# Kernel optimization log

Measured on AMD Instinct MI355X. Metric: run time of the kernel, lower is better.

## Reference

```python
import jax, jax.numpy as jnp
import numpy as np

DIM = 1024
MULTIPLE_OF = 256
NUM_EXPERTS = 8
TOP_K = 2
T = 2048  # flattened tokens


def _hidden_dim(dim: int, multiple_of: int) -> int:
    h = 4 * dim
    h = int(2 * h / 3)
    return multiple_of * ((h + multiple_of - 1) // multiple_of)

HIDDEN = _hidden_dim(DIM, MULTIPLE_OF)  # 2816


def setup_inputs() -> dict:
    key = jax.random.key(0)
    k_x, k_idx, k1, k2, k3 = jax.random.split(key, 5)
    x = jax.random.normal(k_x, (T, DIM), dtype=jnp.float32)
    expert_indices = jax.random.randint(k_idx, (T, TOP_K), 0, NUM_EXPERTS, dtype=jnp.int32)
    # parameters, matching nn.Parameter(torch.randn(E, H, D))
    w1 = jax.random.normal(k1, (NUM_EXPERTS, HIDDEN, DIM), dtype=jnp.float32)
    w2 = jax.random.normal(k2, (NUM_EXPERTS, HIDDEN, DIM), dtype=jnp.float32)
    w3 = jax.random.normal(k3, (NUM_EXPERTS, HIDDEN, DIM), dtype=jnp.float32)
    return {"x": x, "expert_indices": expert_indices, "w1": w1, "w2": w2, "w3": w3}


def reference(x, expert_indices, w1, w2, w3):
    # Same math as the torch module, but instead of materializing the
    # per-token gathered weights [T, A, H, D] (which the original does and
    # which blows up memory), we compute the SwiGLU FFN for ALL experts via
    # dense GEMMs and gather the selected experts' outputs per token.
    # Gather commutes with the per-expert linear maps, so math is identical.
    x1_all = jax.nn.silu(jnp.einsum('td,ehd->teh', x, w1))  # [T, E, H]
    x3_all = jnp.einsum('td,ehd->teh', x, w3)               # [T, E, H]
    g_all = x1_all * x3_all                                  # [T, E, H]
    out_all = jnp.einsum('teh,ehd->ted', g_all, w2)          # [T, E, D]
    # select top_k experts per token -> [T, A, D]
    idx = expert_indices[:, :, None].astype(jnp.int32)       # [T, A, 1]
    return jnp.take_along_axis(out_all, idx, axis=1)
```

## Files before the change

kernel.cpp:

```cpp
#include <hip/hip_runtime.h>

#define NTOK 2048
#define NEXP 8
#define TOPK 2
#define NITEM 4096
#define DIM 1024
#define HID 2816
#define CAP 4096
#define LDP 72

typedef unsigned short u16;
typedef __bf16 bf16x8 __attribute__((ext_vector_type(8)));
typedef float f32x4 __attribute__((ext_vector_type(4)));

__device__ __forceinline__ u16 f2bf(float f) {
  unsigned u = __float_as_uint(f);
  return (u16)((u + 0x7FFFu + ((u >> 16) & 1u)) >> 16);
}
__device__ __forceinline__ unsigned pk2(float a, float b) {
  return (unsigned)f2bf(a) | ((unsigned)f2bf(b) << 16);
}
__device__ __forceinline__ void async16(const void* g, void* l) {
  __builtin_amdgcn_global_load_lds(
      (const __attribute__((address_space(1))) unsigned int*)g,
      (__attribute__((address_space(3))) unsigned int*)l, 16, 0, 0);
}
__device__ __forceinline__ const bf16x8* fragp(const u16* base, int row, int ko) {
  int byte = ((row << 7) + (ko << 1)) ^ ((row & 7) << 4);
  return (const bf16x8*)((const char*)base + byte);
}

__global__ void zero8(int* counts) {
  if (threadIdx.x < NEXP) counts[threadIdx.x] = 0;
}

__global__ void bucket(const int* __restrict__ ei, int* counts, int* lists) {
  int item = blockIdx.x * 256 + threadIdx.x;
  if (item < NITEM) {
    int e = ei[item] & 7;
    int pos = atomicAdd(&counts[e], 1);
    if (pos < CAP) lists[e * CAP + pos] = item;
  }
}

__global__ __launch_bounds__(256) void cvt8(const float* __restrict__ src,
                                            u16* __restrict__ dst, int n8) {
  int i = blockIdx.x * 256 + threadIdx.x;
  if (i >= n8) return;
  float4 v0 = *(const float4*)(src + (size_t)i * 8);
  float4 v1 = *(const float4*)(src + (size_t)i * 8 + 4);
  uint4 u;
  u.x = pk2(v0.x, v0.y); u.y = pk2(v0.z, v0.w);
  u.z = pk2(v1.x, v1.y); u.w = pk2(v1.z, v1.w);
  *(uint4*)(dst + (size_t)i * 8) = u;
}

__global__ __launch_bounds__(256) void tw2(const float* __restrict__ w2, u16* __restrict__ w2t) {
  __shared__ float tile[64][65];
  const int e = blockIdx.z;
  const int h0 = blockIdx.y * 64;
  const int d0 = blockIdx.x * 64;
  const int tid = threadIdx.x;
  const int r = tid >> 4, c = (tid & 15) * 4;
  const float* src = w2 + (size_t)e * HID * DIM;
#pragma unroll
  for (int p = 0; p < 4; ++p) {
    float4 v = *(const float4*)(src + (size_t)(h0 + p * 16 + r) * DIM + d0 + c);
    tile[p * 16 + r][c] = v.x;
    tile[p * 16 + r][c + 1] = v.y;
    tile[p * 16 + r][c + 2] = v.z;
    tile[p * 16 + r][c + 3] = v.w;
  }
  __syncthreads();
  u16* dst = w2t + (size_t)e * DIM * HID;
#pragma unroll
  for (int p = 0; p < 4; ++p) {
    int dd = p * 16 + r;
    uint2 pkv;
    pkv.x = pk2(tile[c][dd], tile[c + 1][dd]);
    pkv.y = pk2(tile[c + 2][dd], tile[c + 3][dd]);
    *(uint2*)(dst + (size_t)(d0 + dd) * HID + h0 + c) = pkv;
  }
}


__global__ __launch_bounds__(256, 2) void gemm1A(
    const u16* __restrict__ xb, const u16* __restrict__ w1b,
    const u16* __restrict__ w3b, const int* __restrict__ counts,
    const int* __restrict__ lists, u16* __restrict__ G) {
  __shared__ __align__(16) u16 As[128 * 64];
  __shared__ __align__(16) u16 B1s[128 * 64];
  __shared__ __align__(16) u16 B3s[128 * 64];
  __shared__ int toks[128];

  const int e = blockIdx.z;
  int cnt = counts[e];
  if ((unsigned)cnt > CAP) cnt = 0;
  const int m0 = blockIdx.y * 128;
  if (m0 >= cnt) return;
  const int n0 = blockIdx.x * 128;
  const int tid = threadIdx.x;

  if (tid < 128) {
    int r = m0 + tid;
    int it = lists[e * CAP + (r < cnt ? r : 0)];
    toks[tid] = ((unsigned)it < NITEM) ? it : 0;
  }
  __syncthreads();

  const int lane = tid & 63;
  const int wr = ((tid >> 7) & 1) * 64;
  const int wc = ((tid >> 6) & 1) * 64;
  const int lr = lane & 15;
  const int kg = lane >> 4;

  const int srow = tid >> 3;
  const int csw = ((tid & 7) ^ (srow & 7)) * 8;

  const u16* xsrc[4];
#pragma unroll
  for (int p = 0; p < 4; ++p)
    xsrc[p] = xb + (size_t)(toks[p * 32 + srow] >> 1) * DIM + csw;
  const u16* b1src = w1b + ((size_t)e * HID + n0 + srow) * DIM + csw;
  const u16* b3src = w3b + ((size_t)e * HID + n0 + srow) * DIM + csw;

  char* aD = (char*)As + tid * 16;
  char* b1D = (char*)B1s + tid * 16;
  char* b3D = (char*)B3s + tid * 16;

  f32x4 acc1[4][4] = {};
  f32x4 acc3[4][4] = {};

  for (int k0 = 0; k0 < DIM; k0 += 64) {
#pragma unroll
    for (int p = 0; p < 4; ++p) {
      async16(xsrc[p] + k0, aD + p * 4096);
      async16(b1src + (size_t)(p * 32) * DIM + k0, b1D + p * 4096);
      async16(b3src + (size_t)(p * 32) * DIM + k0, b3D + p * 4096);
    }
    __syncthreads();
#pragma unroll
    for (int kk = 0; kk < 2; ++kk) {
      const int ko = kk * 32 + kg * 8;
      bf16x8 a[4];
#pragma unroll
      for (int m = 0; m < 4; ++m) a[m] = *fragp(As, wr + m * 16 + lr, ko);
#pragma unroll
      for (int n = 0; n < 4; ++n) {
        bf16x8 b1 = *fragp(B1s, wc + n * 16 + lr, ko);
        bf16x8 b3 = *fragp(B3s, wc + n * 16 + lr, ko);
#pragma unroll
        for (int m = 0; m < 4; ++m) {
          acc1[m][n] = __builtin_amdgcn_mfma_f32_16x16x32_bf16(a[m], b1, acc1[m][n], 0, 0, 0);
          acc3[m][n] = __builtin_amdgcn_mfma_f32_16x16x32_bf16(a[m], b3, acc3[m][n], 0, 0, 0);
        }
      }
    }
    __syncthreads();
  }

#pragma unroll
  for (int m = 0; m < 4; ++m) {
#pragma unroll
    for (int r = 0; r < 4; ++r) {
      const int row = wr + m * 16 + kg * 4 + r;
      if (m0 + row < cnt) {
        const int it = toks[row];
        u16* gp = G + (size_t)it * HID + n0 + wc + lr;
#pragma unroll
        for (int n = 0; n < 4; ++n) {
          float v1 = acc1[m][n][r];
          float v3 = acc3[m][n][r];
          float s = v1 / (1.f + __expf(-v1)) * v3;
          gp[n * 16] = f2bf(s);
        }
      }
    }
  }
}

__global__ __launch_bounds__(256) void gemm2A(
    const u16* __restrict__ G, const u16* __restrict__ w2t,
    const int* __restrict__ counts, const int* __restrict__ lists,
    float* __restrict__ out) {
  __shared__ __align__(16) u16 As[64 * 64];
  __shared__ __align__(16) u16 Bs[64 * 64];
  __shared__ int toks[64];

  const int e = blockIdx.z;
  int cnt = counts[e];
  if ((unsigned)cnt > CAP) cnt = 0;
  const int m0 = blockIdx.y * 64;
  if (m0 >= cnt) return;
  const int n0 = blockIdx.x * 64;
  const int tid = threadIdx.x;

  if (tid < 64) {
    int r = m0 + tid;
    int it = lists[e * CAP + (r < cnt ? r : 0)];
    toks[tid] = ((unsigned)it < NITEM) ? it : 0;
  }
  __syncthreads();

  const int lane = tid & 63;
  const int wr = ((tid >> 7) & 1) * 32;
  const int wc = ((tid >> 6) & 1) * 32;
  const int lr = lane & 15;
  const int kg = lane >> 4;

  const int srow = tid >> 3;
  const int csw = ((tid & 7) ^ (srow & 7)) * 8;

  const u16* asrc[2];
#pragma unroll
  for (int p = 0; p < 2; ++p)
    asrc[p] = G + (size_t)toks[p * 32 + srow] * HID + csw;
  const u16* bsrc = w2t + ((size_t)e * DIM + n0 + srow) * HID + csw;

  char* aD = (char*)As + tid * 16;
  char* bD = (char*)Bs + tid * 16;

  f32x4 acc[2][2] = {};

  for (int k0 = 0; k0 < HID; k0 += 64) {
#pragma unroll
    for (int p = 0; p < 2; ++p) {
      async16(asrc[p] + k0, aD + p * 4096);
      async16(bsrc + (size_t)(p * 32) * HID + k0, bD + p * 4096);
    }
    __syncthreads();
#pragma unroll
    for (int kk = 0; kk < 2; ++kk) {
      const int ko = kk * 32 + kg * 8;
      bf16x8 a[2], b[2];
#pragma unroll
      for (int m = 0; m < 2; ++m) a[m] = *fragp(As, wr + m * 16 + lr, ko);
#pragma unroll
      for (int n = 0; n < 2; ++n) b[n] = *fragp(Bs, wc + n * 16 + lr, ko);
#pragma unroll
      for (int n = 0; n < 2; ++n)
#pragma unroll
        for (int m = 0; m < 2; ++m)
          acc[m][n] = __builtin_amdgcn_mfma_f32_16x16x32_bf16(a[m], b[n], acc[m][n], 0, 0, 0);
    }
    __syncthreads();
  }

#pragma unroll
  for (int m = 0; m < 2; ++m) {
#pragma unroll
    for (int r = 0; r < 4; ++r) {
      const int row = wr + m * 16 + kg * 4 + r;
      if (m0 + row < cnt) {
        const int it = toks[row];
        float* op = out + (size_t)it * DIM + n0 + wc + lr;
#pragma unroll
        for (int n = 0; n < 2; ++n)
          op[n * 16] = acc[m][n][r];
      }
    }
  }
}


__global__ __launch_bounds__(256, 2) void gemm1B(
    const float* __restrict__ x, const float* __restrict__ w1,
    const float* __restrict__ w3, const int* __restrict__ counts,
    const int* __restrict__ lists, u16* __restrict__ G) {
  __shared__ __align__(16) u16 As[128 * LDP];
  __shared__ __align__(16) u16 B1s[128 * LDP];
  __shared__ __align__(16) u16 B3s[128 * LDP];
  __shared__ int toks[128];

  const int e = blockIdx.z;
  int cnt = counts[e];
  if ((unsigned)cnt > CAP) cnt = 0;
  const int m0 = blockIdx.y * 128;
  if (m0 >= cnt) return;
  const int n0 = blockIdx.x * 128;
  const int tid = threadIdx.x;

  if (tid < 128) {
    int r = m0 + tid;
    int it = lists[e * CAP + (r < cnt ? r : 0)];
    toks[tid] = ((unsigned)it < NITEM) ? it : 0;
  }
  __syncthreads();

  const int lane = tid & 63;
  const int wr = ((tid >> 7) & 1) * 64;
  const int wc = ((tid >> 6) & 1) * 64;
  const int lr = lane & 15;
  const int kg = lane >> 4;
  const int arow = tid >> 3;
  const int c8 = (tid & 7) * 8;

  const float* xsrc[4];
#pragma unroll
  for (int p = 0; p < 4; ++p)
    xsrc[p] = x + (size_t)(toks[p * 32 + arow] >> 1) * DIM + c8;
  const float* w1p = w1 + ((size_t)e * HID + n0 + arow) * DIM + c8;
  const float* w3p = w3 + ((size_t)e * HID + n0 + arow) * DIM + c8;

  f32x4 acc1[4][4] = {};
  f32x4 acc3[4][4] = {};

  for (int k0 = 0; k0 < DIM; k0 += 64) {
#pragma unroll
    for (int p = 0; p < 4; ++p) {
      float4 v0 = *(const float4*)(xsrc[p] + k0);
      float4 v1 = *(const float4*)(xsrc[p] + k0 + 4);
      uint4 u;
      u.x = pk2(v0.x, v0.y); u.y = pk2(v0.z, v0.w);
      u.z = pk2(v1.x, v1.y); u.w = pk2(v1.z, v1.w);
      *(uint4*)&As[(p * 32 + arow) * LDP + c8] = u;
    }
#pragma unroll
    for (int p = 0; p < 4; ++p) {
      float4 v0 = *(const float4*)(w1p + (size_t)(p * 32) * DIM + k0);
      float4 v1 = *(const float4*)(w1p + (size_t)(p * 32) * DIM + k0 + 4);
      uint4 u;
      u.x = pk2(v0.x, v0.y); u.y = pk2(v0.z, v0.w);
      u.z = pk2(v1.x, v1.y); u.w = pk2(v1.z, v1.w);
      *(uint4*)&B1s[(p * 32 + arow) * LDP + c8] = u;
      v0 = *(const float4*)(w3p + (size_t)(p * 32) * DIM + k0);
      v1 = *(const float4*)(w3p + (size_t)(p * 32) * DIM + k0 + 4);
      u.x = pk2(v0.x, v0.y); u.y = pk2(v0.z, v0.w);
      u.z = pk2(v1.x, v1.y); u.w = pk2(v1.z, v1.w);
      *(uint4*)&B3s[(p * 32 + arow) * LDP + c8] = u;
    }
    __syncthreads();
#pragma unroll
    for (int kk = 0; kk < 2; ++kk) {
      const int ko = kk * 32 + kg * 8;
      bf16x8 a[4];
#pragma unroll
      for (int m = 0; m < 4; ++m)
        a[m] = *(const bf16x8*)&As[(wr + m * 16 + lr) * LDP + ko];
#pragma unroll
      for (int n = 0; n < 4; ++n) {
        bf16x8 b1 = *(const bf16x8*)&B1s[(wc + n * 16 + lr) * LDP + ko];
        bf16x8 b3 = *(const bf16x8*)&B3s[(wc + n * 16 + lr) * LDP + ko];
#pragma unroll
        for (int m = 0; m < 4; ++m) {
          acc1[m][n] = __builtin_amdgcn_mfma_f32_16x16x32_bf16(a[m], b1, acc1[m][n], 0, 0, 0);
          acc3[m][n] = __builtin_amdgcn_mfma_f32_16x16x32_bf16(a[m], b3, acc3[m][n], 0, 0, 0);
        }
      }
    }
    __syncthreads();
  }

#pragma unroll
  for (int m = 0; m < 4; ++m) {
#pragma unroll
    for (int r = 0; r < 4; ++r) {
      const int row = wr + m * 16 + kg * 4 + r;
      if (m0 + row < cnt) {
        const int it = toks[row];
        u16* gp = G + (size_t)it * HID + n0 + wc + lr;
#pragma unroll
        for (int n = 0; n < 4; ++n) {
          float v1 = acc1[m][n][r];
          float v3 = acc3[m][n][r];
          float s = v1 / (1.f + __expf(-v1)) * v3;
          gp[n * 16] = f2bf(s);
        }
      }
    }
  }
}

__global__ __launch_bounds__(256, 2) void gemm2B(
    const u16* __restrict__ G, const float* __restrict__ w2,
    const int* __restrict__ counts, const int* __restrict__ lists,
    float* __restrict__ out) {
  __shared__ __align__(16) u16 As[128 * LDP];
  __shared__ __align__(16) u16 Bs[128 * LDP];
  __shared__ int toks[128];

  const int e = blockIdx.z;
  int cnt = counts[e];
  if ((unsigned)cnt > CAP) cnt = 0;
  const int m0 = blockIdx.y * 128;
  if (m0 >= cnt) return;
  const int n0 = blockIdx.x * 128;
  const int tid = threadIdx.x;

  if (tid < 128) {
    int r = m0 + tid;
    int it = lists[e * CAP + (r < cnt ? r : 0)];
    toks[tid] = ((unsigned)it < NITEM) ? it : 0;
  }
  __syncthreads();

  const int lane = tid & 63;
  const int wr = ((tid >> 7) & 1) * 64;
  const int wc = ((tid >> 6) & 1) * 64;
  const int lr = lane & 15;
  const int kg = lane >> 4;
  const int arow = tid >> 3;
  const int c8 = (tid & 7) * 8;
  const int brow = tid >> 5;
  const int d4 = (tid & 31) * 4;

  const u16* asrc[4];
#pragma unroll
  for (int p = 0; p < 4; ++p)
    asrc[p] = G + (size_t)toks[p * 32 + arow] * HID + c8;
  const float* bsrc = w2 + ((size_t)e * HID) * DIM + n0 + d4;

  f32x4 acc[4][4] = {};

  for (int k0 = 0; k0 < HID; k0 += 64) {
#pragma unroll
    for (int p = 0; p < 4; ++p) {
      uint4 u = *(const uint4*)(asrc[p] + k0);
      *(uint4*)&As[(p * 32 + arow) * LDP + c8] = u;
    }
#pragma unroll
    for (int p = 0; p < 8; ++p) {
      const int hl = p * 8 + brow;
      float4 v = *(const float4*)(bsrc + (size_t)(k0 + hl) * DIM);
      Bs[(d4 + 0) * LDP + hl] = f2bf(v.x);
      Bs[(d4 + 1) * LDP + hl] = f2bf(v.y);
      Bs[(d4 + 2) * LDP + hl] = f2bf(v.z);
      Bs[(d4 + 3) * LDP + hl] = f2bf(v.w);
    }
    __syncthreads();
#pragma unroll
    for (int kk = 0; kk < 2; ++kk) {
      const int ko = kk * 32 + kg * 8;
      bf16x8 a[4];
#pragma unroll
      for (int m = 0; m < 4; ++m)
        a[m] = *(const bf16x8*)&As[(wr + m * 16 + lr) * LDP + ko];
#pragma unroll
      for (int n = 0; n < 4; ++n) {
        bf16x8 b = *(const bf16x8*)&Bs[(wc + n * 16 + lr) * LDP + ko];
#pragma unroll
        for (int m = 0; m < 4; ++m)
          acc[m][n] = __builtin_amdgcn_mfma_f32_16x16x32_bf16(a[m], b, acc[m][n], 0, 0, 0);
      }
    }
    __syncthreads();
  }

#pragma unroll
  for (int m = 0; m < 4; ++m) {
#pragma unroll
    for (int r = 0; r < 4; ++r) {
      const int row = wr + m * 16 + kg * 4 + r;
      if (m0 + row < cnt) {
        const int it = toks[row];
        float* op = out + (size_t)it * DIM + n0 + wc + lr;
#pragma unroll
        for (int n = 0; n < 4; ++n)
          op[n * 16] = acc[m][n][r];
      }
    }
  }
}

extern "C" void kernel_launch(void* const* d_in, const int* in_sizes, int n_in,
                              void* d_out, int out_size, void* d_ws, size_t ws_size,
                              hipStream_t stream) {
  (void)in_sizes; (void)n_in; (void)out_size;
  const float* x  = (const float*)d_in[0];
  const int*   ei = (const int*)d_in[1];
  const float* w1 = (const float*)d_in[2];
  const float* w2 = (const float*)d_in[3];
  const float* w3 = (const float*)d_in[4];
  float* out = (float*)d_out;

  char* ws = (char*)d_ws;

  const size_t oG = 0;
  const size_t oXB = 23068672u;
  const size_t oW1 = oXB + 4194304u;
  const size_t oW3 = oW1 + 46137344u;
  const size_t oW2T = oW3 + 46137344u;
  const size_t oCNT = oW2T + 46137344u;
  const size_t oLST = oCNT + 64u;
  const size_t needA = oLST + 131072u;

  if (ws_size >= needA) {
    u16* G      = (u16*)(ws + oG);
    u16* xb     = (u16*)(ws + oXB);
    u16* w1b    = (u16*)(ws + oW1);
    u16* w3b    = (u16*)(ws + oW3);
    u16* w2t    = (u16*)(ws + oW2T);
    int* counts = (int*)(ws + oCNT);
    int* lists  = (int*)(ws + oLST);

    zero8<<<1, 64, 0, stream>>>(counts);
    bucket<<<NITEM / 256, 256, 0, stream>>>(ei, counts, lists);
    cvt8<<<(NTOK * DIM / 8) / 256, 256, 0, stream>>>(x, xb, NTOK * DIM / 8);
    cvt8<<<(NEXP * HID * DIM / 8) / 256, 256, 0, stream>>>(w1, w1b, NEXP * HID * DIM / 8);
    cvt8<<<(NEXP * HID * DIM / 8) / 256, 256, 0, stream>>>(w3, w3b, NEXP * HID * DIM / 8);
    tw2<<<dim3(DIM / 64, HID / 64, NEXP), 256, 0, stream>>>(w2, w2t);
    gemm1A<<<dim3(HID / 128, CAP / 128, NEXP), 256, 0, stream>>>(xb, w1b, w3b, counts, lists, G);
    gemm2A<<<dim3(DIM / 64, CAP / 64, NEXP), 256, 0, stream>>>(G, w2t, counts, lists, out);
  } else {
    u16* G      = (u16*)ws;
    int* counts = (int*)(ws + 23068672u);
    int* lists  = (int*)(ws + 23068736u);

    zero8<<<1, 64, 0, stream>>>(counts);
    bucket<<<NITEM / 256, 256, 0, stream>>>(ei, counts, lists);
    gemm1B<<<dim3(HID / 128, CAP / 128, NEXP), 256, 0, stream>>>(x, w1, w3, counts, lists, G);
    gemm2B<<<dim3(DIM / 128, CAP / 128, NEXP), 256, 0, stream>>>(G, w2, counts, lists, out);
  }
}
```

Baseline: 240.6 us.

## Remap grouped GEMM grids for XCD locality and enlarge gemm2 M tile

```diff
diff --git a/kernel.cpp b/kernel.cpp
--- a/kernel.cpp
+++ b/kernel.cpp
@@ -93,12 +93,20 @@
   __shared__ __align__(16) u16 B3s[128 * 64];
   __shared__ int toks[128];
 
-  const int e = blockIdx.z;
+  const int flat = blockIdx.x;
+  const int low3 = flat & 7;
+  const int rest = flat >> 3;
+  const int m_id = rest & 31;
+  const int pairq = rest >> 5;
+  const int pair = pairq * 8 + low3;
+  const int e = pair / 22;
+  const int n_id = pair - e * 22;
+
   int cnt = counts[e];
   if ((unsigned)cnt > CAP) cnt = 0;
-  const int m0 = blockIdx.y * 128;
+  const int m0 = m_id * 128;
   if (m0 >= cnt) return;
-  const int n0 = blockIdx.x * 128;
+  const int n0 = n_id * 128;
   const int tid = threadIdx.x;
 
   if (tid < 128) {
@@ -183,19 +191,27 @@
     const u16* __restrict__ G, const u16* __restrict__ w2t,
     const int* __restrict__ counts, const int* __restrict__ lists,
     float* __restrict__ out) {
-  __shared__ __align__(16) u16 As[64 * 64];
+  __shared__ __align__(16) u16 As[128 * 64];
   __shared__ __align__(16) u16 Bs[64 * 64];
-  __shared__ int toks[64];
-
-  const int e = blockIdx.z;
+  __shared__ int toks[128];
+
+  const int flat = blockIdx.x;
+  const int low3 = flat & 7;
+  const int rest = flat >> 3;
+  const int m_id = rest & 31;
+  const int pairq = rest >> 5;
+  const int pair = pairq * 8 + low3;
+  const int e = pair >> 4;
+  const int n_id = pair & 15;
+
   int cnt = counts[e];
   if ((unsigned)cnt > CAP) cnt = 0;
-  const int m0 = blockIdx.y * 64;
+  const int m0 = m_id * 128;
   if (m0 >= cnt) return;
-  const int n0 = blockIdx.x * 64;
+  const int n0 = n_id * 64;
   const int tid = threadIdx.x;
 
-  if (tid < 64) {
+  if (tid < 128) {
     int r = m0 + tid;
     int it = lists[e * CAP + (r < cnt ? r : 0)];
     toks[tid] = ((unsigned)it < NITEM) ? it : 0;
@@ -203,51 +219,53 @@
   __syncthreads();
 
   const int lane = tid & 63;
-  const int wr = ((tid >> 7) & 1) * 32;
-  const int wc = ((tid >> 6) & 1) * 32;
+  const int wid = tid >> 6;
+  const int wr = (wid >> 1) * 64;
+  const int wc = (wid & 1) * 32;
   const int lr = lane & 15;
   const int kg = lane >> 4;
 
   const int srow = tid >> 3;
   const int csw = ((tid & 7) ^ (srow & 7)) * 8;
 
-  const u16* asrc[2];
-#pragma unroll
-  for (int p = 0; p < 2; ++p)
+  const u16* asrc[4];
+#pragma unroll
+  for (int p = 0; p < 4; ++p)
     asrc[p] = G + (size_t)toks[p * 32 + srow] * HID + csw;
   const u16* bsrc = w2t + ((size_t)e * DIM + n0 + srow) * HID + csw;
 
   char* aD = (char*)As + tid * 16;
   char* bD = (char*)Bs + tid * 16;
 
-  f32x4 acc[2][2] = {};
+  f32x4 acc[4][2] = {};
 
   for (int k0 = 0; k0 < HID; k0 += 64) {
 #pragma unroll
-    for (int p = 0; p < 2; ++p) {
+    for (int p = 0; p < 4; ++p)
       async16(asrc[p] + k0, aD + p * 4096);
+#pragma unroll
+    for (int p = 0; p < 2; ++p)
       async16(bsrc + (size_t)(p * 32) * HID + k0, bD + p * 4096);
-    }
     __syncthreads();
 #pragma unroll
     for (int kk = 0; kk < 2; ++kk) {
       const int ko = kk * 32 + kg * 8;
-      bf16x8 a[2], b[2];
-#pragma unroll
-      for (int m = 0; m < 2; ++m) a[m] = *fragp(As, wr + m * 16 + lr, ko);
+      bf16x8 a[4], b[2];
+#pragma unroll
+      for (int m = 0; m < 4; ++m) a[m] = *fragp(As, wr + m * 16 + lr, ko);
 #pragma unroll
       for (int n = 0; n < 2; ++n) b[n] = *fragp(Bs, wc + n * 16 + lr, ko);
 #pragma unroll
       for (int n = 0; n < 2; ++n)
 #pragma unroll
-        for (int m = 0; m < 2; ++m)
+        for (int m = 0; m < 4; ++m)
           acc[m][n] = __builtin_amdgcn_mfma_f32_16x16x32_bf16(a[m], b[n], acc[m][n], 0, 0, 0);
     }
     __syncthreads();
   }
 
 #pragma unroll
-  for (int m = 0; m < 2; ++m) {
+  for (int m = 0; m < 4; ++m) {
 #pragma unroll
     for (int r = 0; r < 4; ++r) {
       const int row = wr + m * 16 + kg * 4 + r;
@@ -499,8 +517,8 @@
     cvt8<<<(NEXP * HID * DIM / 8) / 256, 256, 0, stream>>>(w1, w1b, NEXP * HID * DIM / 8);
     cvt8<<<(NEXP * HID * DIM / 8) / 256, 256, 0, stream>>>(w3, w3b, NEXP * HID * DIM / 8);
     tw2<<<dim3(DIM / 64, HID / 64, NEXP), 256, 0, stream>>>(w2, w2t);
-    gemm1A<<<dim3(HID / 128, CAP / 128, NEXP), 256, 0, stream>>>(xb, w1b, w3b, counts, lists, G);
-    gemm2A<<<dim3(DIM / 64, CAP / 64, NEXP), 256, 0, stream>>>(G, w2t, counts, lists, out);
+    gemm1A<<<8 * 22 * 32, 256, 0, stream>>>(xb, w1b, w3b, counts, lists, G);
+    gemm2A<<<8 * 16 * 32, 256, 0, stream>>>(G, w2t, counts, lists, out);
   } else {
     u16* G      = (u16*)ws;
     int* counts = (int*)(ws + 23068672u);
```

After: 257.7 us. +7.1%, slower.

## Double-buffer LDS tiles with BK=32 in both GEMMs and enlarge gemm2 tiles

Applied to the files above, without the earlier changes.

```diff
diff --git a/kernel.cpp b/kernel.cpp
--- a/kernel.cpp
+++ b/kernel.cpp
@@ -25,8 +25,8 @@
       (const __attribute__((address_space(1))) unsigned int*)g,
       (__attribute__((address_space(3))) unsigned int*)l, 16, 0, 0);
 }
-__device__ __forceinline__ const bf16x8* fragp(const u16* base, int row, int ko) {
-  int byte = ((row << 7) + (ko << 1)) ^ ((row & 7) << 4);
+__device__ __forceinline__ const bf16x8* fragp32(const u16* base, int row, int kg) {
+  int byte = (row << 6) + (((kg << 4) ^ ((row & 3) << 4)));
   return (const bf16x8*)((const char*)base + byte);
 }
 
@@ -88,9 +88,9 @@
     const u16* __restrict__ xb, const u16* __restrict__ w1b,
     const u16* __restrict__ w3b, const int* __restrict__ counts,
     const int* __restrict__ lists, u16* __restrict__ G) {
-  __shared__ __align__(16) u16 As[128 * 64];
-  __shared__ __align__(16) u16 B1s[128 * 64];
-  __shared__ __align__(16) u16 B3s[128 * 64];
+  __shared__ __align__(16) u16 As[2][128 * 32];
+  __shared__ __align__(16) u16 B1s[2][128 * 32];
+  __shared__ __align__(16) u16 B3s[2][128 * 32];
   __shared__ int toks[128];
 
   const int e = blockIdx.z;
@@ -114,50 +114,61 @@
   const int lr = lane & 15;
   const int kg = lane >> 4;
 
-  const int srow = tid >> 3;
-  const int csw = ((tid & 7) ^ (srow & 7)) * 8;
-
-  const u16* xsrc[4];
-#pragma unroll
-  for (int p = 0; p < 4; ++p)
-    xsrc[p] = xb + (size_t)(toks[p * 32 + srow] >> 1) * DIM + csw;
-  const u16* b1src = w1b + ((size_t)e * HID + n0 + srow) * DIM + csw;
-  const u16* b3src = w3b + ((size_t)e * HID + n0 + srow) * DIM + csw;
-
-  char* aD = (char*)As + tid * 16;
-  char* b1D = (char*)B1s + tid * 16;
-  char* b3D = (char*)B3s + tid * 16;
+  const int prow = tid >> 2;
+  const int scol = ((tid & 3) ^ (prow & 3)) * 8;
+
+  const u16* xs0 = xb + (size_t)(toks[prow] >> 1) * DIM + scol;
+  const u16* xs1 = xb + (size_t)(toks[64 + prow] >> 1) * DIM + scol;
+  const u16* b1a = w1b + ((size_t)e * HID + n0 + prow) * DIM + scol;
+  const u16* b1b = b1a + (size_t)64 * DIM;
+  const u16* b3a = w3b + ((size_t)e * HID + n0 + prow) * DIM + scol;
+  const u16* b3b = b3a + (size_t)64 * DIM;
+
+  const int doff = tid * 16;
 
   f32x4 acc1[4][4] = {};
   f32x4 acc3[4][4] = {};
 
-  for (int k0 = 0; k0 < DIM; k0 += 64) {
-#pragma unroll
-    for (int p = 0; p < 4; ++p) {
-      async16(xsrc[p] + k0, aD + p * 4096);
-      async16(b1src + (size_t)(p * 32) * DIM + k0, b1D + p * 4096);
-      async16(b3src + (size_t)(p * 32) * DIM + k0, b3D + p * 4096);
+#define STG1(buf, k)                                             \
+  {                                                              \
+    char* aD = (char*)As[buf] + doff;                            \
+    char* d1 = (char*)B1s[buf] + doff;                           \
+    char* d3 = (char*)B3s[buf] + doff;                           \
+    async16(xs0 + (k), aD);                                      \
+    async16(xs1 + (k), aD + 4096);                               \
+    async16(b1a + (k), d1);                                      \
+    async16(b1b + (k), d1 + 4096);                               \
+    async16(b3a + (k), d3);                                      \
+    async16(b3b + (k), d3 + 4096);                               \
+  }
+
+  STG1(0, 0);
+  __syncthreads();
+
+  int cur = 0;
+  for (int k0 = 0; k0 < DIM; k0 += 32) {
+    const int nk = k0 + 32;
+    if (nk < DIM) STG1(cur ^ 1, nk);
+    const u16* Ab = As[cur];
+    const u16* B1b_ = B1s[cur];
+    const u16* B3b_ = B3s[cur];
+    bf16x8 a[4];
+#pragma unroll
+    for (int m = 0; m < 4; ++m) a[m] = *fragp32(Ab, wr + m * 16 + lr, kg);
+#pragma unroll
+    for (int n = 0; n < 4; ++n) {
+      bf16x8 b1 = *fragp32(B1b_, wc + n * 16 + lr, kg);
+      bf16x8 b3 = *fragp32(B3b_, wc + n * 16 + lr, kg);
+#pragma unroll
+      for (int m = 0; m < 4; ++m) {
+        acc1[m][n] = __builtin_amdgcn_mfma_f32_16x16x32_bf16(a[m], b1, acc1[m][n], 0, 0, 0);
+        acc3[m][n] = __builtin_amdgcn_mfma_f32_16x16x32_bf16(a[m], b3, acc3[m][n], 0, 0, 0);
+      }
     }
     __syncthreads();
-#pragma unroll
-    for (int kk = 0; kk < 2; ++kk) {
-      const int ko = kk * 32 + kg * 8;
-      bf16x8 a[4];
-#pragma unroll
-      for (int m = 0; m < 4; ++m) a[m] = *fragp(As, wr + m * 16 + lr, ko);
-#pragma unroll
-      for (int n = 0; n < 4; ++n) {
-        bf16x8 b1 = *fragp(B1s, wc + n * 16 + lr, ko);
-        bf16x8 b3 = *fragp(B3s, wc + n * 16 + lr, ko);
-#pragma unroll
-        for (int m = 0; m < 4; ++m) {
-          acc1[m][n] = __builtin_amdgcn_mfma_f32_16x16x32_bf16(a[m], b1, acc1[m][n], 0, 0, 0);
-          acc3[m][n] = __builtin_amdgcn_mfma_f32_16x16x32_bf16(a[m], b3, acc3[m][n], 0, 0, 0);
-        }
-      }
-    }
-    __syncthreads();
-  }
+    cur ^= 1;
+  }
+#undef STG1
 
 #pragma unroll
   for (int m = 0; m < 4; ++m) {
@@ -179,23 +190,23 @@
   }
 }
 
-__global__ __launch_bounds__(256) void gemm2A(
+__global__ __launch_bounds__(256, 2) void gemm2A(
     const u16* __restrict__ G, const u16* __restrict__ w2t,
     const int* __restrict__ counts, const int* __restrict__ lists,
     float* __restrict__ out) {
-  __shared__ __align__(16) u16 As[64 * 64];
-  __shared__ __align__(16) u16 Bs[64 * 64];
-  __shared__ int toks[64];
+  __shared__ __align__(16) u16 As[2][128 * 32];
+  __shared__ __align__(16) u16 Bs[2][128 * 32];
+  __shared__ int toks[128];
 
   const int e = blockIdx.z;
   int cnt = counts[e];
   if ((unsigned)cnt > CAP) cnt = 0;
-  const int m0 = blockIdx.y * 64;
+  const int m0 = blockIdx.y * 128;
   if (m0 >= cnt) return;
-  const int n0 = blockIdx.x * 64;
+  const int n0 = blockIdx.x * 128;
   const int tid = threadIdx.x;
 
-  if (tid < 64) {
+  if (tid < 128) {
     int r = m0 + tid;
     int it = lists[e * CAP + (r < cnt ? r : 0)];
     toks[tid] = ((unsigned)it < NITEM) ? it : 0;
@@ -203,51 +214,59 @@
   __syncthreads();
 
   const int lane = tid & 63;
-  const int wr = ((tid >> 7) & 1) * 32;
-  const int wc = ((tid >> 6) & 1) * 32;
+  const int wr = ((tid >> 7) & 1) * 64;
+  const int wc = ((tid >> 6) & 1) * 64;
   const int lr = lane & 15;
   const int kg = lane >> 4;
 
-  const int srow = tid >> 3;
-  const int csw = ((tid & 7) ^ (srow & 7)) * 8;
-
-  const u16* asrc[2];
-#pragma unroll
-  for (int p = 0; p < 2; ++p)
-    asrc[p] = G + (size_t)toks[p * 32 + srow] * HID + csw;
-  const u16* bsrc = w2t + ((size_t)e * DIM + n0 + srow) * HID + csw;
-
-  char* aD = (char*)As + tid * 16;
-  char* bD = (char*)Bs + tid * 16;
-
-  f32x4 acc[2][2] = {};
-
-  for (int k0 = 0; k0 < HID; k0 += 64) {
-#pragma unroll
-    for (int p = 0; p < 2; ++p) {
-      async16(asrc[p] + k0, aD + p * 4096);
-      async16(bsrc + (size_t)(p * 32) * HID + k0, bD + p * 4096);
-    }
+  const int prow = tid >> 2;
+  const int scol = ((tid & 3) ^ (prow & 3)) * 8;
+
+  const u16* as0 = G + (size_t)toks[prow] * HID + scol;
+  const u16* as1 = G + (size_t)toks[64 + prow] * HID + scol;
+  const u16* bs0 = w2t + ((size_t)e * DIM + n0 + prow) * HID + scol;
+  const u16* bs1 = bs0 + (size_t)64 * HID;
+
+  const int doff = tid * 16;
+
+  f32x4 acc[4][4] = {};
+
+#define STG2(buf, k)                       \
+  {                                        \
+    char* aD = (char*)As[buf] + doff;      \
+    char* bD = (char*)Bs[buf] + doff;      \
+    async16(as0 + (k), aD);                \
+    async16(as1 + (k), aD + 4096);         \
+    async16(bs0 + (k), bD);                \
+    async16(bs1 + (k), bD + 4096);         \
+  }
+
+  STG2(0, 0);
+  __syncthreads();
+
+  int cur = 0;
+  for (int k0 = 0; k0 < HID; k0 += 32) {
+    const int nk = k0 + 32;
+    if (nk < HID) STG2(cur ^ 1, nk);
+    const u16* Ab = As[cur];
+    const u16* Bb = Bs[cur];
+    bf16x8 a[4], b[4];
+#pragma unroll
+    for (int m = 0; m < 4; ++m) a[m] = *fragp32(Ab, wr + m * 16 + lr, kg);
+#pragma unroll
+    for (int n = 0; n < 4; ++n) b[n] = *fragp32(Bb, wc + n * 16 + lr, kg);
+#pragma unroll
+    for (int n = 0; n < 4; ++n)
+#pragma unroll
+      for (int m = 0; m < 4; ++m)
+        acc[m][n] = __builtin_amdgcn_mfma_f32_16x16x32_bf16(a[m], b[n], acc[m][n], 0, 0, 0);
     __syncthreads();
-#pragma unroll
-    for (int kk = 0; kk < 2; ++kk) {
-      const int ko = kk * 32 + kg * 8;
-      bf16x8 a[2], b[2];
-#pragma unroll
-      for (int m = 0; m < 2; ++m) a[m] = *fragp(As, wr + m * 16 + lr, ko);
-#pragma unroll
-      for (int n = 0; n < 2; ++n) b[n] = *fragp(Bs, wc + n * 16 + lr, ko);
-#pragma unroll
-      for (int n = 0; n < 2; ++n)
-#pragma unroll
-        for (int m = 0; m < 2; ++m)
-          acc[m][n] = __builtin_amdgcn_mfma_f32_16x16x32_bf16(a[m], b[n], acc[m][n], 0, 0, 0);
-    }
-    __syncthreads();
-  }
-
-#pragma unroll
-  for (int m = 0; m < 2; ++m) {
+    cur ^= 1;
+  }
+#undef STG2
+
+#pragma unroll
+  for (int m = 0; m < 4; ++m) {
 #pragma unroll
     for (int r = 0; r < 4; ++r) {
       const int row = wr + m * 16 + kg * 4 + r;
@@ -255,7 +274,7 @@
         const int it = toks[row];
         float* op = out + (size_t)it * DIM + n0 + wc + lr;
 #pragma unroll
-        for (int n = 0; n < 2; ++n)
+        for (int n = 0; n < 4; ++n)
           op[n * 16] = acc[m][n][r];
       }
     }
@@ -500,7 +519,7 @@
     cvt8<<<(NEXP * HID * DIM / 8) / 256, 256, 0, stream>>>(w3, w3b, NEXP * HID * DIM / 8);
     tw2<<<dim3(DIM / 64, HID / 64, NEXP), 256, 0, stream>>>(w2, w2t);
     gemm1A<<<dim3(HID / 128, CAP / 128, NEXP), 256, 0, stream>>>(xb, w1b, w3b, counts, lists, G);
-    gemm2A<<<dim3(DIM / 64, CAP / 64, NEXP), 256, 0, stream>>>(G, w2t, counts, lists, out);
+    gemm2A<<<dim3(DIM / 128, CAP / 128, NEXP), 256, 0, stream>>>(G, w2t, counts, lists, out);
   } else {
     u16* G      = (u16*)ws;
     int* counts = (int*)(ws + 23068672u);
```

Result: slower. 287.0 us (+19.3%).
